# Kernel optimization log

Measured on AMD Instinct MI355X. Metric: run time of the kernel, lower is better.

The kernel has to match this reference:

```python
import jax, jax.numpy as jnp
import numpy as np
import math

D = 1024
H = 16
HD = D // H
P = 64  # bias_proj_dim
B, N, M = 4, 1024, 2048
EPS_LN = 1e-5
EPS_NORM = 1e-12


def _ln(x, g, b):
    mu = jnp.mean(x, axis=-1, keepdims=True)
    var = jnp.var(x, axis=-1, keepdims=True)
    return (x - mu) * jax.lax.rsqrt(var + EPS_LN) * g + b


def _l2norm_dim1(x):
    # torch F.normalize(x, p=2) default dim=1 -> normalize over the sequence axis
    n = jnp.sqrt(jnp.sum(x * x, axis=1, keepdims=True))
    return x / jnp.maximum(n, EPS_NORM)


def setup_inputs() -> dict:
    key = jax.random.key(0)
    ks = jax.random.split(key, 16)
    s = 1.0 / math.sqrt(D)
    inp = {
        'dataset_features': jax.random.normal(ks[0], (B, N, D), jnp.float32),
        'visual_features': jax.random.normal(ks[1], (B, M, D), jnp.float32),
        # linear weights stored as (in, out): y = x @ W + b
        'wq_w': jax.random.normal(ks[2], (D, D), jnp.float32) * s,
        'wq_b': jnp.zeros((D,), jnp.float32),
        'wk_w': jax.random.normal(ks[3], (D, D), jnp.float32) * s,
        'wk_b': jnp.zeros((D,), jnp.float32),
        'wv_w': jax.random.normal(ks[4], (D, D), jnp.float32) * s,
        'wv_b': jnp.zeros((D,), jnp.float32),
        'wo_w': jax.random.normal(ks[5], (D, D), jnp.float32) * s,
        'wo_b': jnp.zeros((D,), jnp.float32),
        'gq_w': jax.random.normal(ks[6], (D, P), jnp.float32) * s,
        'gq_b': jnp.zeros((P,), jnp.float32),
        'gk_w': jax.random.normal(ks[7], (D, P), jnp.float32) * s,
        'gk_b': jnp.zeros((P,), jnp.float32),
        'pos_scale': jnp.asarray(2.0, jnp.float32),
        'neg_scale': jnp.asarray(50.0, jnp.float32),
        'attn_logit_scale': jnp.asarray(math.log(10.0), jnp.float32),
        'ln_q_g': jnp.ones((D,), jnp.float32),
        'ln_q_b': jnp.zeros((D,), jnp.float32),
        'ln_kv_g': jnp.ones((D,), jnp.float32),
        'ln_kv_b': jnp.zeros((D,), jnp.float32),
        'ln_out_g': jnp.ones((D,), jnp.float32),
        'ln_out_b': jnp.zeros((D,), jnp.float32),
        'ff1_w': jax.random.normal(ks[8], (D, 2 * D), jnp.float32) * s,
        'ff1_b': jnp.zeros((2 * D,), jnp.float32),
        'ff2_w': jax.random.normal(ks[9], (2 * D, D), jnp.float32) * (1.0 / math.sqrt(2 * D)),
        'ff2_b': jnp.zeros((D,), jnp.float32),
    }
    return inp


def reference(dataset_features, visual_features, wq_w, wq_b, wk_w, wk_b, wv_w, wv_b,
              wo_w, wo_b, gq_w, gq_b, gk_w, gk_b, pos_scale, neg_scale,
              attn_logit_scale, ln_q_g, ln_q_b, ln_kv_g, ln_kv_b, ln_out_g, ln_out_b,
              ff1_w, ff1_b, ff2_w, ff2_b):
    residual = dataset_features
    q_in = _ln(dataset_features, ln_q_g, ln_q_b)   # [B,N,D]
    kv_in = _ln(visual_features, ln_kv_g, ln_kv_b)  # [B,M,D]

    geo_q = _l2norm_dim1(q_in @ gq_w + gq_b)   # [B,N,P], normalized over N
    geo_k = _l2norm_dim1(kv_in @ gk_w + gk_b)  # [B,M,P], normalized over M
    bias_raw = jnp.einsum('bnp,bmp->bnm', geo_q, geo_k)  # [B,N,M]
    full_bias = jax.nn.relu(bias_raw) * pos_scale - jax.nn.relu(-bias_raw) * neg_scale

    q = (q_in @ wq_w + wq_b).reshape(B, N, H, HD).transpose(0, 2, 1, 3)   # [B,H,N,hd]
    k = (kv_in @ wk_w + wk_b).reshape(B, M, H, HD).transpose(0, 2, 1, 3)  # [B,H,M,hd]
    v = (kv_in @ wv_w + wv_b).reshape(B, M, H, HD).transpose(0, 2, 1, 3)

    logits = jnp.einsum('bhnd,bhmd->bhnm', q, k) / math.sqrt(HD)
    logits = logits * jnp.exp(attn_logit_scale)
    scores = logits + full_bias[:, None, :, :]
    attn = jax.nn.softmax(scores, axis=-1)
    out = jnp.einsum('bhnm,bhmd->bhnd', attn, v).transpose(0, 2, 1, 3).reshape(B, N, D)
    out = out @ wo_w + wo_b
    out = residual + out

    residual = out
    h = _ln(out, ln_out_g, ln_out_b)
    ff = jax.nn.gelu(h @ ff1_w + ff1_b, approximate=False) @ ff2_w + ff2_b
    return residual + ff
```

## Files before the change

kernel.cpp:

```cpp
#include <hip/hip_runtime.h>


typedef __bf16 bf16x8 __attribute__((ext_vector_type(8)));
typedef __bf16 bf16x4 __attribute__((ext_vector_type(4)));
typedef float  f32x4  __attribute__((ext_vector_type(4)));

__device__ inline f32x4 mfma16(bf16x8 a, bf16x8 b, f32x4 c) {
  return __builtin_amdgcn_mfma_f32_16x16x32_bf16(a, b, c, 0, 0, 0);
}

__device__ inline f32x4 mfma16k16(bf16x4 a, bf16x4 b, f32x4 c) {
  f32x4 d;
  asm("v_mfma_f32_16x16x16_bf16 %0, %1, %2, %3"
      : "=v"(d) : "v"(a), "v"(b), "v"(c));
  return d;
}

__device__ inline void glds16(const void* g, void* l) {
  __builtin_amdgcn_global_load_lds(
      (const __attribute__((address_space(1))) void*)g,
      (__attribute__((address_space(3))) void*)l, 16, 0, 0);
}

__device__ inline int swz(int row, int col) {
  return row * 64 + ((((col >> 3) ^ (row & 7)) << 3) | (col & 7));
}

#define DB 1024
#define DH 16
#define DHD 64
#define DP 64
#define NB 4
#define NN 1024
#define NM 2048

__global__ __launch_bounds__(256) void k_transpose_all(
    const float* __restrict__ w0, const float* __restrict__ w1,
    const float* __restrict__ w2, const float* __restrict__ w3,
    const float* __restrict__ f1, const float* __restrict__ f2,
    const float* __restrict__ g0, const float* __restrict__ g1,
    __bf16* __restrict__ o0, __bf16* __restrict__ o1,
    __bf16* __restrict__ o2, __bf16* __restrict__ o3,
    __bf16* __restrict__ of1, __bf16* __restrict__ of2,
    __bf16* __restrict__ og0, __bf16* __restrict__ og1) {
  __shared__ float tile[32][33];
  int id = blockIdx.x;
  const float* in;
  __bf16* out;
  int K, O, x, y;
  if (id < 4096) {
    int mi = id >> 10, r = id & 1023;
    in = mi == 0 ? w0 : mi == 1 ? w1 : mi == 2 ? w2 : w3;
    out = mi == 0 ? o0 : mi == 1 ? o1 : mi == 2 ? o2 : o3;
    K = 1024; O = 1024; x = r & 31; y = r >> 5;
  } else if (id < 6144) {
    int r = id - 4096; in = f1; out = of1; K = 1024; O = 2048; x = r & 63; y = r >> 6;
  } else if (id < 8192) {
    int r = id - 6144; in = f2; out = of2; K = 2048; O = 1024; x = r & 31; y = r >> 5;
  } else if (id < 8256) {
    int r = id - 8192; in = g0; out = og0; K = 1024; O = 64; x = r & 1; y = r >> 1;
  } else {
    int r = id - 8256; in = g1; out = og1; K = 1024; O = 64; x = r & 1; y = r >> 1;
  }
  int k0 = y * 32, o0c = x * 32;
  int tx = threadIdx.x & 31, ty = threadIdx.x >> 5;
#pragma unroll
  for (int r = ty; r < 32; r += 8)
    tile[r][tx] = in[(size_t)(k0 + r) * O + (o0c + tx)];
  __syncthreads();
#pragma unroll
  for (int r = ty; r < 32; r += 8)
    out[(size_t)(o0c + r) * K + (k0 + tx)] = (__bf16)tile[tx][r];
}

__device__ inline void ln_body(const float* __restrict__ x,
                               const float* __restrict__ g,
                               const float* __restrict__ bb,
                               __bf16* __restrict__ y, size_t row) {
  int t = threadIdx.x;
  float4 v = ((const float4*)(x + row * 1024))[t];
  float s = v.x + v.y + v.z + v.w;
  float ss = v.x * v.x + v.y * v.y + v.z * v.z + v.w * v.w;
#pragma unroll
  for (int o = 32; o; o >>= 1) {
    s += __shfl_down(s, o, 64);
    ss += __shfl_down(ss, o, 64);
  }
  __shared__ float r1[4], r2[4];
  if ((t & 63) == 0) { r1[t >> 6] = s; r2[t >> 6] = ss; }
  __syncthreads();
  s = r1[0] + r1[1] + r1[2] + r1[3];
  ss = r2[0] + r2[1] + r2[2] + r2[3];
  float mu = s * (1.f / 1024.f);
  float rstd = rsqrtf(ss * (1.f / 1024.f) - mu * mu + 1e-5f);
  float4 gv = ((const float4*)g)[t];
  float4 bv = ((const float4*)bb)[t];
  __bf16* yr = y + row * 1024 + t * 4;
  yr[0] = (__bf16)((v.x - mu) * rstd * gv.x + bv.x);
  yr[1] = (__bf16)((v.y - mu) * rstd * gv.y + bv.y);
  yr[2] = (__bf16)((v.z - mu) * rstd * gv.z + bv.z);
  yr[3] = (__bf16)((v.w - mu) * rstd * gv.w + bv.w);
}

__global__ __launch_bounds__(256) void k_layernorm(
    const float* __restrict__ x, const float* __restrict__ g,
    const float* __restrict__ bb, __bf16* __restrict__ y) {
  ln_body(x, g, bb, y, blockIdx.x);
}

__global__ __launch_bounds__(256) void k_layernorm2(
    const float* __restrict__ x1, const float* __restrict__ g1,
    const float* __restrict__ b1, __bf16* __restrict__ y1,
    const float* __restrict__ x2, const float* __restrict__ g2,
    const float* __restrict__ b2, __bf16* __restrict__ y2) {
  int row = blockIdx.x;
  if (row < 4096) ln_body(x1, g1, b1, y1, row);
  else ln_body(x2, g2, b2, y2, row - 4096);
}

__global__ __launch_bounds__(256) void k_geo(
    const __bf16* __restrict__ qin, const __bf16* __restrict__ kvin,
    const __bf16* __restrict__ gqw, const __bf16* __restrict__ gkw,
    const float* __restrict__ gqb, const float* __restrict__ gkb,
    __bf16* __restrict__ geoq, __bf16* __restrict__ geok) {
  const int blk = blockIdx.x;
  const bool isq = blk < 128;
  const __bf16* A = isq ? qin : kvin;
  const __bf16* Bt = isq ? gqw : gkw;
  const float* bias = isq ? gqb : gkb;
  __bf16* C = isq ? geoq : geok;
  const int row0 = (isq ? blk : blk - 128) * 32;
  __shared__ __align__(16) __bf16 As[32][72], Bs[64][72];
  const int t = threadIdx.x, lane = t & 63, w = t >> 6;
  const int quad = lane >> 4, l15 = lane & 15;
  const int wr = w >> 1, wc = w & 1;
  const int sr = t >> 3, skc = (t & 7) * 8;
  const __bf16* aP = A + (size_t)(row0 + sr) * 1024 + skc;
  const __bf16* bP0 = Bt + (size_t)sr * 1024 + skc;
  const __bf16* bP1 = Bt + (size_t)(sr + 32) * 1024 + skc;
  bf16x8 av = *(const bf16x8*)aP;
  bf16x8 bv0 = *(const bf16x8*)bP0;
  bf16x8 bv1 = *(const bf16x8*)bP1;
  f32x4 acc[2] = {};
  for (int k0 = 0; k0 < 1024; k0 += 64) {
    __syncthreads();
    *(bf16x8*)&As[sr][skc] = av;
    *(bf16x8*)&Bs[sr][skc] = bv0;
    *(bf16x8*)&Bs[sr + 32][skc] = bv1;
    __syncthreads();
    if (k0 + 64 < 1024) {
      av = *(const bf16x8*)(aP + k0 + 64);
      bv0 = *(const bf16x8*)(bP0 + k0 + 64);
      bv1 = *(const bf16x8*)(bP1 + k0 + 64);
    }
#pragma unroll
    for (int ks = 0; ks < 2; ks++) {
      bf16x8 af = *(const bf16x8*)&As[wr * 16 + l15][ks * 32 + quad * 8];
#pragma unroll
      for (int ct = 0; ct < 2; ct++) {
        bf16x8 bfr = *(const bf16x8*)&Bs[wc * 32 + ct * 16 + l15][ks * 32 + quad * 8];
        acc[ct] = mfma16(af, bfr, acc[ct]);
      }
    }
  }
#pragma unroll
  for (int ct = 0; ct < 2; ct++) {
    int col = wc * 32 + ct * 16 + l15;
    float bc = bias[col];
#pragma unroll
    for (int i = 0; i < 4; i++) {
      int row = row0 + wr * 16 + quad * 4 + i;
      C[(size_t)row * 64 + col] = (__bf16)(acc[ct][i] + bc);
    }
  }
}

__global__ __launch_bounds__(256) void k_l2sum(
    const __bf16* __restrict__ gq, const __bf16* __restrict__ gk,
    float* __restrict__ sums) {
  int chunk = blockIdx.x, b = blockIdx.y, z = blockIdx.z;
  if (z == 0 && chunk >= 8) return;
  const __bf16* src = z ? gk : gq;
  int rows = z ? 2048 : 1024;
  const unsigned* base = (const unsigned*)(src + (size_t)b * rows * 64) + chunk * 128 * 32;
  int t = threadIdx.x, c = t & 31, ro = t >> 5;
  float s0 = 0.f, s1 = 0.f;
  for (int r = ro; r < 128; r += 8) {
    unsigned u = base[r * 32 + c];
    float f0 = __uint_as_float(u << 16);
    float f1 = __uint_as_float(u & 0xffff0000u);
    s0 += f0 * f0;
    s1 += f1 * f1;
  }
  __shared__ float ls[64];
  if (t < 64) ls[t] = 0.f;
  __syncthreads();
  atomicAdd(&ls[c * 2], s0);
  atomicAdd(&ls[c * 2 + 1], s1);
  __syncthreads();
  if (t < 64) atomicAdd(&sums[z * 256 + b * 64 + t], ls[t]);
}

__global__ __launch_bounds__(256) void k_l2scale(
    __bf16* __restrict__ gk, const float* __restrict__ sums) {
  int chunk = blockIdx.x, b = blockIdx.y;
  unsigned* base = (unsigned*)(gk + (size_t)b * 2048 * 64) + chunk * 128 * 32;
  int t = threadIdx.x, c = t & 31, ro = t >> 5;
  float sq0 = sums[b * 64 + c * 2], sq1 = sums[b * 64 + c * 2 + 1];
  float sk0 = sums[256 + b * 64 + c * 2], sk1 = sums[256 + b * 64 + c * 2 + 1];
  float m0 = 1.f / (fmaxf(sqrtf(sq0), 1e-12f) * fmaxf(sqrtf(sk0), 1e-12f));
  float m1 = 1.f / (fmaxf(sqrtf(sq1), 1e-12f) * fmaxf(sqrtf(sk1), 1e-12f));
  for (int r = ro; r < 128; r += 8) {
    unsigned u = base[r * 32 + c];
    float f0 = __uint_as_float(u << 16) * m0;
    float f1 = __uint_as_float(u & 0xffff0000u) * m1;
    unsigned short h0 = __builtin_bit_cast(unsigned short, (__bf16)f0);
    unsigned short h1 = __builtin_bit_cast(unsigned short, (__bf16)f1);
    base[r * 32 + c] = (unsigned)h0 | ((unsigned)h1 << 16);
  }
}

__global__ __launch_bounds__(256) void k_bias(
    const __bf16* __restrict__ gq, const __bf16* __restrict__ gk,
    const float* __restrict__ psc, const float* __restrict__ nsc,
    __bf16* __restrict__ Bias) {
  const int mt0 = blockIdx.x * 128, nt0 = blockIdx.y * 128, b = blockIdx.z;
  const int t = threadIdx.x, lane = t & 63, w = t >> 6;
  const int quad = lane >> 4, l15 = lane & 15;
  const int wm = w & 1, wn = w >> 1;
  const float LOG2E = 1.44269504089f;
  const float pos2 = psc[0] * LOG2E, neg2 = nsc[0] * LOG2E;
  const __bf16* gqb = gq + (size_t)(b * NN + nt0 + wn * 64) * DP;
  const __bf16* gkb = gk + (size_t)(b * NM + mt0 + wm * 64) * DP;
  bf16x8 af[4][2], bg[4][2];
#pragma unroll
  for (int i = 0; i < 4; i++)
#pragma unroll
    for (int ks = 0; ks < 2; ks++) {
      af[i][ks] = *(const bf16x8*)(gkb + (size_t)(i * 16 + l15) * DP + ks * 32 + quad * 8);
      bg[i][ks] = *(const bf16x8*)(gqb + (size_t)(i * 16 + l15) * DP + ks * 32 + quad * 8);
    }
  __bf16* ob = Bias + (size_t)(b * NN + nt0 + wn * 64) * NM + mt0 + wm * 64;
#pragma unroll
  for (int nt = 0; nt < 4; nt++)
#pragma unroll
    for (int mt = 0; mt < 4; mt++) {
      f32x4 acc = {};
      acc = mfma16(af[mt][0], bg[nt][0], acc);
      acc = mfma16(af[mt][1], bg[nt][1], acc);
      bf16x4 o;
#pragma unroll
      for (int i = 0; i < 4; i++) {
        float x = acc[i];
        o[i] = (__bf16)(x > 0.f ? x * pos2 : x * neg2);
      }
      *(bf16x4*)(ob + (size_t)(nt * 16 + l15) * NM + mt * 16 + quad * 4) = o;
    }
}

__global__ __launch_bounds__(256, 4) void k_qkv(
    const __bf16* __restrict__ qin, const __bf16* __restrict__ kvin,
    const __bf16* __restrict__ twq, const __bf16* __restrict__ twk,
    const __bf16* __restrict__ twv, const float* __restrict__ qbias,
    const float* __restrict__ kbias, const float* __restrict__ vbias,
    __bf16* __restrict__ qb, __bf16* __restrict__ kb, __bf16* __restrict__ vtb) {
  int id = blockIdx.x;
  const __bf16 *A, *Bt;
  const float* bias;
  __bf16* C;
  int my, nx, Ndim;
  bool rowbias;
  if (id < 256) {
    A = qin; Bt = twq; bias = qbias; C = qb;
    nx = id & 7; my = id >> 3; Ndim = 1024; rowbias = false;
  } else if (id < 768) {
    id -= 256;
    A = kvin; Bt = twk; bias = kbias; C = kb;
    nx = id & 7; my = id >> 3; Ndim = 1024; rowbias = false;
  } else {
    id -= 768;
    A = twv; Bt = kvin; bias = vbias; C = vtb;
    nx = id & 63; my = id >> 6; Ndim = 8192; rowbias = true;
  }
  const int Kdim = 1024;
  __shared__ __align__(16) __bf16 As[128 * 32];
  __shared__ __align__(16) __bf16 Bs[128 * 32];
  const int m0 = my * 128, n0 = nx * 128;
  const int t = threadIdx.x, lane = t & 63, w = t >> 6;
  const int quad = lane >> 4, l15 = lane & 15;
  const int wr = w >> 1, wc = w & 1;
  const int srow = lane >> 2, scol = (lane & 3) * 8;
  const __bf16* aS0 = A + (size_t)(m0 + w * 32 + srow) * Kdim + scol;
  const __bf16* bS0 = Bt + (size_t)(n0 + w * 32 + srow) * Kdim + scol;
  const size_t K16 = (size_t)16 * Kdim;
  __bf16* lA0 = &As[(w * 32) * 32];
  __bf16* lB0 = &Bs[(w * 32) * 32];

  f32x4 acc[4][4] = {};
  for (int k0 = 0; k0 < Kdim; k0 += 32) {
    __syncthreads();
    glds16(aS0 + k0, lA0);
    glds16(aS0 + K16 + k0, lA0 + 16 * 32);
    glds16(bS0 + k0, lB0);
    glds16(bS0 + K16 + k0, lB0 + 16 * 32);
    __syncthreads();
    bf16x8 af[4], bg[4];
#pragma unroll
    for (int rt = 0; rt < 4; rt++)
      af[rt] = *(const bf16x8*)&As[(wr * 64 + rt * 16 + l15) * 32 + quad * 8];
#pragma unroll
    for (int ct = 0; ct < 4; ct++)
      bg[ct] = *(const bf16x8*)&Bs[(wc * 64 + ct * 16 + l15) * 32 + quad * 8];
#pragma unroll
    for (int rt = 0; rt < 4; rt++)
#pragma unroll
      for (int ct = 0; ct < 4; ct++)
        acc[rt][ct] = mfma16(af[rt], bg[ct], acc[rt][ct]);
  }
#pragma unroll
  for (int rt = 0; rt < 4; rt++) {
    int row = m0 + wr * 64 + rt * 16 + quad * 4;
#pragma unroll
    for (int ct = 0; ct < 4; ct++) {
      int col = n0 + wc * 64 + ct * 16 + l15;
      float bcol = rowbias ? 0.f : bias[col];
#pragma unroll
      for (int i = 0; i < 4; i++) {
        float vv = acc[rt][ct][i] + (rowbias ? bias[row + i] : bcol);
        C[(size_t)(row + i) * Ndim + col] = (__bf16)vv;
      }
    }
  }
}

__global__ __launch_bounds__(256, 3) void k_gemm128g(
    const __bf16* __restrict__ A, const __bf16* __restrict__ Bt,
    const float* __restrict__ bias, __bf16* __restrict__ Cout,
    int Ndim, int Kdim) {
  __shared__ __align__(16) __bf16 As[128 * 32];
  __shared__ __align__(16) __bf16 Bs[128 * 32];
  const int m0 = blockIdx.y * 128, n0 = blockIdx.x * 128;
  const int t = threadIdx.x, lane = t & 63, w = t >> 6;
  const int quad = lane >> 4, l15 = lane & 15;
  const int wr = w >> 1, wc = w & 1;
  const int srow = lane >> 2, scol = (lane & 3) * 8;
  const __bf16* aS0 = A + (size_t)(m0 + w * 32 + srow) * Kdim + scol;
  const __bf16* bS0 = Bt + (size_t)(n0 + w * 32 + srow) * Kdim + scol;
  const size_t K16 = (size_t)16 * Kdim;
  __bf16* lA0 = &As[(w * 32) * 32];
  __bf16* lB0 = &Bs[(w * 32) * 32];

  f32x4 acc[4][4] = {};
  for (int k0 = 0; k0 < Kdim; k0 += 32) {
    __syncthreads();
    glds16(aS0 + k0, lA0);
    glds16(aS0 + K16 + k0, lA0 + 16 * 32);
    glds16(bS0 + k0, lB0);
    glds16(bS0 + K16 + k0, lB0 + 16 * 32);
    __syncthreads();
    bf16x8 af[4], bg[4];
#pragma unroll
    for (int rt = 0; rt < 4; rt++)
      af[rt] = *(const bf16x8*)&As[(wr * 64 + rt * 16 + l15) * 32 + quad * 8];
#pragma unroll
    for (int ct = 0; ct < 4; ct++)
      bg[ct] = *(const bf16x8*)&Bs[(wc * 64 + ct * 16 + l15) * 32 + quad * 8];
#pragma unroll
    for (int rt = 0; rt < 4; rt++)
#pragma unroll
      for (int ct = 0; ct < 4; ct++)
        acc[rt][ct] = mfma16(af[rt], bg[ct], acc[rt][ct]);
  }
#pragma unroll
  for (int rt = 0; rt < 4; rt++) {
    int row = m0 + wr * 64 + rt * 16 + quad * 4;
#pragma unroll
    for (int ct = 0; ct < 4; ct++) {
      int col = n0 + wc * 64 + ct * 16 + l15;
      float bcol = bias[col];
#pragma unroll
      for (int i = 0; i < 4; i++) {
        float vv = acc[rt][ct][i] + bcol;
        Cout[(size_t)(row + i) * Ndim + col] =
            (__bf16)(0.5f * vv * (1.f + erff(vv * 0.70710678118f)));
      }
    }
  }
}

__global__ __launch_bounds__(256, 2) void k_gemmn64(
    const __bf16* __restrict__ A, const __bf16* __restrict__ Bt,
    const float* __restrict__ bias, const float* __restrict__ resid,
    float* __restrict__ Cout, int Ndim, int Kdim) {
  __shared__ __align__(16) __bf16 As[128 * 32];
  __shared__ __align__(16) __bf16 Bs[64 * 32];
  const int m0 = blockIdx.y * 128, n0 = blockIdx.x * 64;
  const int t = threadIdx.x, lane = t & 63, w = t >> 6;
  const int quad = lane >> 4, l15 = lane & 15;
  const int wr = w >> 1, wc = w & 1;
  const int srow = lane >> 2, scol = (lane & 3) * 8;
  const __bf16* aS0 = A + (size_t)(m0 + w * 32 + srow) * Kdim + scol;
  const __bf16* bS0 = Bt + (size_t)(n0 + w * 16 + srow) * Kdim + scol;
  const size_t K16 = (size_t)16 * Kdim;
  __bf16* lA0 = &As[(w * 32) * 32];
  __bf16* lB0 = &Bs[(w * 16) * 32];

  f32x4 acc[4][2] = {};
  for (int k0 = 0; k0 < Kdim; k0 += 32) {
    __syncthreads();
    glds16(aS0 + k0, lA0);
    glds16(aS0 + K16 + k0, lA0 + 16 * 32);
    glds16(bS0 + k0, lB0);
    __syncthreads();
    bf16x8 af[4], bg[2];
#pragma unroll
    for (int rt = 0; rt < 4; rt++)
      af[rt] = *(const bf16x8*)&As[(wr * 64 + rt * 16 + l15) * 32 + quad * 8];
#pragma unroll
    for (int ct = 0; ct < 2; ct++)
      bg[ct] = *(const bf16x8*)&Bs[(wc * 32 + ct * 16 + l15) * 32 + quad * 8];
#pragma unroll
    for (int rt = 0; rt < 4; rt++)
#pragma unroll
      for (int ct = 0; ct < 2; ct++)
        acc[rt][ct] = mfma16(af[rt], bg[ct], acc[rt][ct]);
  }
#pragma unroll
  for (int rt = 0; rt < 4; rt++) {
    int row = m0 + wr * 64 + rt * 16 + quad * 4;
#pragma unroll
    for (int ct = 0; ct < 2; ct++) {
      int col = n0 + wc * 32 + ct * 16 + l15;
      float bcol = bias[col];
#pragma unroll
      for (int i = 0; i < 4; i++) {
        size_t idx = (size_t)(row + i) * Ndim + col;
        Cout[idx] = acc[rt][ct][i] + bcol + resid[idx];
      }
    }
  }
}

__global__ __launch_bounds__(256, 4) void k_flash(
    const __bf16* __restrict__ Q, const __bf16* __restrict__ K,
    const __bf16* __restrict__ Vt, const __bf16* __restrict__ Bias,
    const float* __restrict__ als, __bf16* __restrict__ Out) {
  const int o = blockIdx.x;
  const int bh = o & 63, x = o >> 6;
  const int b = bh & 3, h = bh >> 2;
  const int t = threadIdx.x, w = t >> 6, lane = t & 63;
  const int quad = lane >> 4, l15 = lane & 15;
  const int qh = w >> 1, mh = w & 1;
  const int row0 = x * 64 + qh * 32;
  const float sc2 = __expf(als[0]) * 0.125f * 1.44269504089f;

  __shared__ __align__(16) __bf16 smem[16384];
  __shared__ float Lred[2][64];

  const __bf16* Qb = Q + (size_t)(b * NN + row0) * DB + h * DHD;
  const __bf16* Kb = K + (size_t)b * NM * DB + h * DHD;
  const __bf16* Vb = Vt + (size_t)(h * DHD) * (NB * NM) + (size_t)b * NM;
  const __bf16* Bb = Bias + (size_t)(b * NN + row0) * NM + mh * 32;

  const int r0 = t >> 3, gc = (t & 7) * 8;
  const int sw0 = swz(r0, gc), sw1 = sw0 + 32 * 64;
  const int r1 = r0 + 32;

  bf16x8 qf[2][2];
#pragma unroll
  for (int rt = 0; rt < 2; rt++)
#pragma unroll
    for (int ks = 0; ks < 2; ks++)
      qf[rt][ks] = *(const bf16x8*)(Qb + (size_t)(rt * 16 + l15) * DB + ks * 32 + quad * 8);

  {
    bf16x8 k0v = *(const bf16x8*)(Kb + (size_t)r0 * DB + gc);
    bf16x8 k1v = *(const bf16x8*)(Kb + (size_t)r1 * DB + gc);
    bf16x8 v0v = *(const bf16x8*)(Vb + (size_t)r0 * (NB * NM) + gc);
    bf16x8 v1v = *(const bf16x8*)(Vb + (size_t)r1 * (NB * NM) + gc);
    *(bf16x8*)&smem[sw0] = k0v;
    *(bf16x8*)&smem[sw1] = k1v;
    *(bf16x8*)&smem[4096 + sw0] = v0v;
    *(bf16x8*)&smem[4096 + sw1] = v1v;
  }

  float lrowq[2] = {};
  f32x4 oacc[2][4] = {};
  f32x4 z4 = {0.f, 0.f, 0.f, 0.f};

  for (int it = 0; it < 32; ++it) {
    const int m0 = it * 64;
    const int cur = it & 1;
    __syncthreads();
    bf16x4 btv[2][2];
#pragma unroll
    for (int ct = 0; ct < 2; ct++)
#pragma unroll
      for (int rt = 0; rt < 2; rt++)
        btv[ct][rt] = *(const bf16x4*)(Bb + (size_t)(rt * 16 + l15) * NM +
                                       m0 + ct * 16 + quad * 4);
    bf16x8 kn0, kn1, vn0, vn1;
    if (it + 1 < 32) {
      kn0 = *(const bf16x8*)(Kb + (size_t)(m0 + 64 + r0) * DB + gc);
      kn1 = *(const bf16x8*)(Kb + (size_t)(m0 + 64 + r1) * DB + gc);
      vn0 = *(const bf16x8*)(Vb + (size_t)r0 * (NB * NM) + m0 + 64 + gc);
      vn1 = *(const bf16x8*)(Vb + (size_t)r1 * (NB * NM) + m0 + 64 + gc);
    }
    const __bf16* Kcur = smem + cur * 8192;
    const __bf16* Vcur = Kcur + 4096;
    bf16x8 kf[2][2];
#pragma unroll
    for (int ct = 0; ct < 2; ct++)
#pragma unroll
      for (int ks = 0; ks < 2; ks++)
        kf[ct][ks] = *(const bf16x8*)&Kcur[swz(mh * 32 + ct * 16 + l15, ks * 32 + quad * 8)];
    bf16x4 p[2][2];
#pragma unroll
    for (int ct = 0; ct < 2; ct++)
#pragma unroll
      for (int rt = 0; rt < 2; rt++) {
        f32x4 s = mfma16(kf[ct][1], qf[rt][1], mfma16(kf[ct][0], qf[rt][0], z4));
        bf16x4 pk;
        float part = 0.f;
#pragma unroll
        for (int i = 0; i < 4; i++) {
          float pv = __builtin_amdgcn_exp2f(fmaf(s[i], sc2, (float)btv[ct][rt][i]));
          part += pv;
          pk[i] = (__bf16)pv;
        }
        lrowq[rt] += part;
        p[ct][rt] = pk;
      }
#pragma unroll
    for (int ct = 0; ct < 2; ct++)
#pragma unroll
      for (int dt = 0; dt < 4; dt++) {
        bf16x4 vfr = *(const bf16x4*)&Vcur[swz(dt * 16 + l15, mh * 32 + ct * 16 + quad * 4)];
#pragma unroll
        for (int rt = 0; rt < 2; rt++)
          oacc[rt][dt] = mfma16k16(p[ct][rt], vfr, oacc[rt][dt]);
      }
    if (it + 1 < 32) {
      __bf16* dst = smem + (cur ^ 1) * 8192;
      *(bf16x8*)&dst[sw0] = kn0;
      *(bf16x8*)&dst[sw1] = kn1;
      *(bf16x8*)&dst[4096 + sw0] = vn0;
      *(bf16x8*)&dst[4096 + sw1] = vn1;
    }
  }

  __syncthreads();
  float* Ored = (float*)smem;
  float ltot[2];
#pragma unroll
  for (int rt = 0; rt < 2; rt++) {
    float l = lrowq[rt];
    l += __shfl_xor(l, 16, 64);
    l += __shfl_xor(l, 32, 64);
    ltot[rt] = l;
  }
  if (quad == 0) {
    Lred[mh][qh * 32 + l15] = ltot[0];
    Lred[mh][qh * 32 + 16 + l15] = ltot[1];
  }
  if (mh == 1) {
#pragma unroll
    for (int rt = 0; rt < 2; rt++)
#pragma unroll
      for (int dt = 0; dt < 4; dt++)
#pragma unroll
        for (int i = 0; i < 4; i++)
          Ored[(qh * 32 + rt * 16 + quad * 4 + i) * 64 + dt * 16 + l15] =
              oacc[rt][dt][i];
  }
  __syncthreads();
  if (mh == 0) {
#pragma unroll
    for (int rt = 0; rt < 2; rt++)
#pragma unroll
      for (int i = 0; i < 4; i++) {
        int r = qh * 32 + rt * 16 + quad * 4 + i;
        float inv = 1.f / (Lred[0][r] + Lred[1][r]);
#pragma unroll
        for (int dt = 0; dt < 4; dt++) {
          float val = (oacc[rt][dt][i] + Ored[r * 64 + dt * 16 + l15]) * inv;
          Out[(size_t)(b * NN + x * 64 + r) * DB + h * DHD + dt * 16 + l15] =
              (__bf16)val;
        }
      }
  }
}

extern "C" void kernel_launch(void* const* d_in, const int* in_sizes, int n_in,
                              void* d_out, int out_size, void* d_ws, size_t ws_size,
                              hipStream_t stream) {
  const float* dataset = (const float*)d_in[0];
  const float* visual = (const float*)d_in[1];
  const float* wq_w = (const float*)d_in[2];
  const float* wq_b = (const float*)d_in[3];
  const float* wk_w = (const float*)d_in[4];
  const float* wk_b = (const float*)d_in[5];
  const float* wv_w = (const float*)d_in[6];
  const float* wv_b = (const float*)d_in[7];
  const float* wo_w = (const float*)d_in[8];
  const float* wo_b = (const float*)d_in[9];
  const float* gq_w = (const float*)d_in[10];
  const float* gq_b = (const float*)d_in[11];
  const float* gk_w = (const float*)d_in[12];
  const float* gk_b = (const float*)d_in[13];
  const float* pos_scale = (const float*)d_in[14];
  const float* neg_scale = (const float*)d_in[15];
  const float* als = (const float*)d_in[16];
  const float* ln_q_g = (const float*)d_in[17];
  const float* ln_q_b = (const float*)d_in[18];
  const float* ln_kv_g = (const float*)d_in[19];
  const float* ln_kv_b = (const float*)d_in[20];
  const float* ln_out_g = (const float*)d_in[21];
  const float* ln_out_b = (const float*)d_in[22];
  const float* ff1_w = (const float*)d_in[23];
  const float* ff1_b = (const float*)d_in[24];
  const float* ff2_w = (const float*)d_in[25];
  const float* ff2_b = (const float*)d_in[26];

  char* ws = (char*)d_ws;
  size_t off = 0;
  auto alloc = [&](size_t bytes) {
    size_t o = off;
    off += (bytes + 255) & ~(size_t)255;
    return o;
  };
  __bf16* t_wq = (__bf16*)(ws + alloc((size_t)1024 * 1024 * 2));
  __bf16* t_wk = (__bf16*)(ws + alloc((size_t)1024 * 1024 * 2));
  __bf16* t_wv = (__bf16*)(ws + alloc((size_t)1024 * 1024 * 2));
  __bf16* t_wo = (__bf16*)(ws + alloc((size_t)1024 * 1024 * 2));
  __bf16* t_ff1 = (__bf16*)(ws + alloc((size_t)2048 * 1024 * 2));
  __bf16* t_ff2 = (__bf16*)(ws + alloc((size_t)1024 * 2048 * 2));
  __bf16* t_gq = (__bf16*)(ws + alloc((size_t)64 * 1024 * 2));
  __bf16* t_gk = (__bf16*)(ws + alloc((size_t)64 * 1024 * 2));
  size_t qin_off = alloc((size_t)4096 * 1024 * 2);
  size_t kvin_off = alloc((size_t)8192 * 1024 * 2);
  __bf16* qin = (__bf16*)(ws + qin_off);
  __bf16* kvin = (__bf16*)(ws + kvin_off);
  __bf16* geoq = (__bf16*)(ws + alloc((size_t)4096 * 64 * 2));
  __bf16* geok = (__bf16*)(ws + alloc((size_t)8192 * 64 * 2));
  float* sums = (float*)(ws + alloc((size_t)2 * 4 * 64 * 4));
  __bf16* biasb = (__bf16*)(ws + alloc((size_t)4096 * 2048 * 2));
  __bf16* qb = (__bf16*)(ws + alloc((size_t)4096 * 1024 * 2));
  __bf16* kb = (__bf16*)(ws + alloc((size_t)8192 * 1024 * 2));
  __bf16* vtb = (__bf16*)(ws + alloc((size_t)1024 * 8192 * 2));
  __bf16* attn = (__bf16*)(ws + alloc((size_t)4096 * 1024 * 2));
  __bf16* ffh = (__bf16*)(ws + alloc((size_t)4096 * 2048 * 2));
  float* out1 = (float*)(ws + kvin_off);
  __bf16* hbuf = (__bf16*)(ws + qin_off);
  float* outp = (float*)d_out;

  dim3 blk(256);
  k_transpose_all<<<8320, blk, 0, stream>>>(wq_w, wk_w, wv_w, wo_w, ff1_w, ff2_w,
                                            gq_w, gk_w, t_wq, t_wk, t_wv, t_wo,
                                            t_ff1, t_ff2, t_gq, t_gk);
  k_layernorm2<<<12288, blk, 0, stream>>>(dataset, ln_q_g, ln_q_b, qin,
                                          visual, ln_kv_g, ln_kv_b, kvin);
  k_geo<<<384, blk, 0, stream>>>(qin, kvin, t_gq, t_gk, gq_b, gk_b, geoq, geok);
  hipMemsetAsync(sums, 0, 2 * 4 * 64 * 4, stream);
  k_l2sum<<<dim3(16, 4, 2), blk, 0, stream>>>(geoq, geok, sums);
  k_l2scale<<<dim3(16, 4), blk, 0, stream>>>(geok, sums);
  k_bias<<<dim3(16, 8, 4), blk, 0, stream>>>(geoq, geok, pos_scale, neg_scale,
                                             biasb);
  k_qkv<<<1280, blk, 0, stream>>>(qin, kvin, t_wq, t_wk, t_wv,
                                  wq_b, wk_b, wv_b, qb, kb, vtb);
  k_flash<<<1024, blk, 0, stream>>>(qb, kb, vtb, biasb, als, attn);
  k_gemmn64<<<dim3(16, 32), blk, 0, stream>>>(attn, t_wo, wo_b, dataset, out1,
                                              1024, 1024);
  k_layernorm<<<4096, blk, 0, stream>>>(out1, ln_out_g, ln_out_b, hbuf);
  k_gemm128g<<<dim3(16, 32), blk, 0, stream>>>(hbuf, t_ff1, ff1_b, ffh,
                                               2048, 1024);
  k_gemmn64<<<dim3(16, 32), blk, 0, stream>>>(ffh, t_ff2, ff2_b, out1, outp,
                                              1024, 2048);
}
```

Baseline: 466.4 us.

## Give each flash wave full key range and swizzle GEMM block order for XCDs

The flash attention kernel now assigns each of the four waves its own 32 query rows across the full 64-key tile. Each block covers 128 query rows, so it launches half as many blocks. This removes the cross-wave split over keys and the shared-memory reduction of partial outputs and row sums at the end, but doubles per-wave register use, and the occupancy hint drops to 2. Separately, the QKV, FF1 and output/FF2 GEMMs remap block IDs so consecutive hardware blocks (spread round-robin over the 8 XCDs) work on neighbouring tiles, aiming for better L2 reuse.

```diff
diff --git a/kernel.cpp b/kernel.cpp
--- a/kernel.cpp
+++ b/kernel.cpp
@@ -264,7 +264,8 @@
     const __bf16* __restrict__ twv, const float* __restrict__ qbias,
     const float* __restrict__ kbias, const float* __restrict__ vbias,
     __bf16* __restrict__ qb, __bf16* __restrict__ kb, __bf16* __restrict__ vtb) {
-  int id = blockIdx.x;
+  int id0 = blockIdx.x;
+  int id = (id0 & 7) * 160 + (id0 >> 3);
   const __bf16 *A, *Bt;
   const float* bias;
   __bf16* C;
@@ -339,7 +340,9 @@
     int Ndim, int Kdim) {
   __shared__ __align__(16) __bf16 As[128 * 32];
   __shared__ __align__(16) __bf16 Bs[128 * 32];
-  const int m0 = blockIdx.y * 128, n0 = blockIdx.x * 128;
+  int p = blockIdx.y * gridDim.x + blockIdx.x;
+  int l = (p & 7) * 64 + (p >> 3);
+  const int m0 = (l >> 4) * 128, n0 = (l & 15) * 128;
   const int t = threadIdx.x, lane = t & 63, w = t >> 6;
   const int quad = lane >> 4, l15 = lane & 15;
   const int wr = w >> 1, wc = w & 1;
@@ -394,7 +397,9 @@
     float* __restrict__ Cout, int Ndim, int Kdim) {
   __shared__ __align__(16) __bf16 As[128 * 32];
   __shared__ __align__(16) __bf16 Bs[64 * 32];
-  const int m0 = blockIdx.y * 128, n0 = blockIdx.x * 64;
+  int p = blockIdx.y * gridDim.x + blockIdx.x;
+  int l = (p & 7) * 64 + (p >> 3);
+  const int m0 = (l >> 4) * 128, n0 = (l & 15) * 64;
   const int t = threadIdx.x, lane = t & 63, w = t >> 6;
   const int quad = lane >> 4, l15 = lane & 15;
   const int wr = w >> 1, wc = w & 1;
@@ -441,7 +446,7 @@
   }
 }
 
-__global__ __launch_bounds__(256, 4) void k_flash(
+__global__ __launch_bounds__(256, 2) void k_flash(
     const __bf16* __restrict__ Q, const __bf16* __restrict__ K,
     const __bf16* __restrict__ Vt, const __bf16* __restrict__ Bias,
     const float* __restrict__ als, __bf16* __restrict__ Out) {
@@ -450,17 +455,15 @@
   const int b = bh & 3, h = bh >> 2;
   const int t = threadIdx.x, w = t >> 6, lane = t & 63;
   const int quad = lane >> 4, l15 = lane & 15;
-  const int qh = w >> 1, mh = w & 1;
-  const int row0 = x * 64 + qh * 32;
+  const int row0 = x * 128 + w * 32;
   const float sc2 = __expf(als[0]) * 0.125f * 1.44269504089f;
 
-  __shared__ __align__(16) __bf16 smem[16384];
-  __shared__ float Lred[2][64];
+  __shared__ __align__(16) __bf16 smem[2][8192];
 
   const __bf16* Qb = Q + (size_t)(b * NN + row0) * DB + h * DHD;
   const __bf16* Kb = K + (size_t)b * NM * DB + h * DHD;
   const __bf16* Vb = Vt + (size_t)(h * DHD) * (NB * NM) + (size_t)b * NM;
-  const __bf16* Bb = Bias + (size_t)(b * NN + row0) * NM + mh * 32;
+  const __bf16* Bb = Bias + (size_t)(b * NN + row0) * NM;
 
   const int r0 = t >> 3, gc = (t & 7) * 8;
   const int sw0 = swz(r0, gc), sw1 = sw0 + 32 * 64;
@@ -478,10 +481,10 @@
     bf16x8 k1v = *(const bf16x8*)(Kb + (size_t)r1 * DB + gc);
     bf16x8 v0v = *(const bf16x8*)(Vb + (size_t)r0 * (NB * NM) + gc);
     bf16x8 v1v = *(const bf16x8*)(Vb + (size_t)r1 * (NB * NM) + gc);
-    *(bf16x8*)&smem[sw0] = k0v;
-    *(bf16x8*)&smem[sw1] = k1v;
-    *(bf16x8*)&smem[4096 + sw0] = v0v;
-    *(bf16x8*)&smem[4096 + sw1] = v1v;
+    *(bf16x8*)&smem[0][sw0] = k0v;
+    *(bf16x8*)&smem[0][sw1] = k1v;
+    *(bf16x8*)&smem[0][4096 + sw0] = v0v;
+    *(bf16x8*)&smem[0][4096 + sw1] = v1v;
   }
 
   float lrowq[2] = {};
@@ -492,9 +495,9 @@
     const int m0 = it * 64;
     const int cur = it & 1;
     __syncthreads();
-    bf16x4 btv[2][2];
-#pragma unroll
-    for (int ct = 0; ct < 2; ct++)
+    bf16x4 btv[4][2];
+#pragma unroll
+    for (int ct = 0; ct < 4; ct++)
 #pragma unroll
       for (int rt = 0; rt < 2; rt++)
         btv[ct][rt] = *(const bf16x4*)(Bb + (size_t)(rt * 16 + l15) * NM +
@@ -506,17 +509,23 @@
       vn0 = *(const bf16x8*)(Vb + (size_t)r0 * (NB * NM) + m0 + 64 + gc);
       vn1 = *(const bf16x8*)(Vb + (size_t)r1 * (NB * NM) + m0 + 64 + gc);
     }
-    const __bf16* Kcur = smem + cur * 8192;
+    const __bf16* Kcur = smem[cur];
     const __bf16* Vcur = Kcur + 4096;
-    bf16x8 kf[2][2];
-#pragma unroll
-    for (int ct = 0; ct < 2; ct++)
+    bf16x8 kf[4][2];
+#pragma unroll
+    for (int ct = 0; ct < 4; ct++)
 #pragma unroll
       for (int ks = 0; ks < 2; ks++)
-        kf[ct][ks] = *(const bf16x8*)&Kcur[swz(mh * 32 + ct * 16 + l15, ks * 32 + quad * 8)];
-    bf16x4 p[2][2];
-#pragma unroll
-    for (int ct = 0; ct < 2; ct++)
+        kf[ct][ks] = *(const bf16x8*)&Kcur[swz(ct * 16 + l15, ks * 32 + quad * 8)];
+    bf16x4 vf[4][4];
+#pragma unroll
+    for (int dt = 0; dt < 4; dt++)
+#pragma unroll
+      for (int ct = 0; ct < 4; ct++)
+        vf[dt][ct] = *(const bf16x4*)&Vcur[swz(dt * 16 + l15, ct * 16 + quad * 4)];
+    bf16x4 p[4][2];
+#pragma unroll
+    for (int ct = 0; ct < 4; ct++)
 #pragma unroll
       for (int rt = 0; rt < 2; rt++) {
         f32x4 s = mfma16(kf[ct][1], qf[rt][1], mfma16(kf[ct][0], qf[rt][0], z4));
@@ -532,16 +541,14 @@
         p[ct][rt] = pk;
       }
 #pragma unroll
-    for (int ct = 0; ct < 2; ct++)
-#pragma unroll
-      for (int dt = 0; dt < 4; dt++) {
-        bf16x4 vfr = *(const bf16x4*)&Vcur[swz(dt * 16 + l15, mh * 32 + ct * 16 + quad * 4)];
+    for (int ct = 0; ct < 4; ct++)
+#pragma unroll
+      for (int dt = 0; dt < 4; dt++)
 #pragma unroll
         for (int rt = 0; rt < 2; rt++)
-          oacc[rt][dt] = mfma16k16(p[ct][rt], vfr, oacc[rt][dt]);
-      }
+          oacc[rt][dt] = mfma16k16(p[ct][rt], vf[dt][ct], oacc[rt][dt]);
     if (it + 1 < 32) {
-      __bf16* dst = smem + (cur ^ 1) * 8192;
+      __bf16* dst = smem[cur ^ 1];
       *(bf16x8*)&dst[sw0] = kn0;
       *(bf16x8*)&dst[sw1] = kn1;
       *(bf16x8*)&dst[4096 + sw0] = vn0;
@@ -549,8 +556,6 @@
     }
   }
 
-  __syncthreads();
-  float* Ored = (float*)smem;
   float ltot[2];
 #pragma unroll
   for (int rt = 0; rt < 2; rt++) {
@@ -559,36 +564,17 @@
     l += __shfl_xor(l, 32, 64);
     ltot[rt] = l;
   }
-  if (quad == 0) {
-    Lred[mh][qh * 32 + l15] = ltot[0];
-    Lred[mh][qh * 32 + 16 + l15] = ltot[1];
-  }
-  if (mh == 1) {
-#pragma unroll
-    for (int rt = 0; rt < 2; rt++)
+#pragma unroll
+  for (int rt = 0; rt < 2; rt++)
+#pragma unroll
+    for (int i = 0; i < 4; i++) {
+      float li = __shfl(ltot[rt], quad * 4 + i, 64);
+      float inv = 1.f / li;
 #pragma unroll
       for (int dt = 0; dt < 4; dt++)
-#pragma unroll
-        for (int i = 0; i < 4; i++)
-          Ored[(qh * 32 + rt * 16 + quad * 4 + i) * 64 + dt * 16 + l15] =
-              oacc[rt][dt][i];
-  }
-  __syncthreads();
-  if (mh == 0) {
-#pragma unroll
-    for (int rt = 0; rt < 2; rt++)
-#pragma unroll
-      for (int i = 0; i < 4; i++) {
-        int r = qh * 32 + rt * 16 + quad * 4 + i;
-        float inv = 1.f / (Lred[0][r] + Lred[1][r]);
-#pragma unroll
-        for (int dt = 0; dt < 4; dt++) {
-          float val = (oacc[rt][dt][i] + Ored[r * 64 + dt * 16 + l15]) * inv;
-          Out[(size_t)(b * NN + x * 64 + r) * DB + h * DHD + dt * 16 + l15] =
-              (__bf16)val;
-        }
-      }
-  }
+        Out[(size_t)(b * NN + row0 + rt * 16 + quad * 4 + i) * DB + h * DHD + dt * 16 + l15] =
+            (__bf16)(oacc[rt][dt][i] * inv);
+    }
 }
 
 extern "C" void kernel_launch(void* const* d_in, const int* in_sizes, int n_in,
@@ -668,7 +654,7 @@
                                              biasb);
   k_qkv<<<1280, blk, 0, stream>>>(qin, kvin, t_wq, t_wk, t_wv,
                                   wq_b, wk_b, wv_b, qb, kb, vtb);
-  k_flash<<<1024, blk, 0, stream>>>(qb, kb, vtb, biasb, als, attn);
+  k_flash<<<512, blk, 0, stream>>>(qb, kb, vtb, biasb, als, attn);
   k_gemmn64<<<dim3(16, 32), blk, 0, stream>>>(attn, t_wo, wo_b, dataset, out1,
                                               1024, 1024);
   k_layernorm<<<4096, blk, 0, stream>>>(out1, ln_out_g, ln_out_b, hbuf);
```

Result: no change. 468.0 us (+0.3%).
